# Kernel tuning notes

Hardware: AMD Instinct MI355X
Metric: run time of the kernel (lower is better)

Reference implementation:

```python
import jax, jax.numpy as jnp
import numpy as np

B, S, D, H, DFF = 2, 2048, 768, 12, 3072
HD = D // H
LN_EPS = 1e-5


def _layernorm(x, g, b):
    mu = jnp.mean(x, axis=-1, keepdims=True)
    var = jnp.mean((x - mu) ** 2, axis=-1, keepdims=True)
    return (x - mu) * jax.lax.rsqrt(var + LN_EPS) * g + b


def setup_inputs() -> dict:
    key = jax.random.key(0)
    ks = jax.random.split(key, 16)
    s_d = 1.0 / np.sqrt(D)
    s_ff = 1.0 / np.sqrt(DFF)
    return {
        "x": jax.random.normal(ks[0], (B, S, D), jnp.float32),
        "alibi_bias": jax.random.normal(ks[1], (H, S, S), jnp.float32) * 0.1,
        "Wq": jax.random.normal(ks[2], (D, D), jnp.float32) * s_d,
        "bq": jnp.zeros((D,), jnp.float32),
        "Wk": jax.random.normal(ks[3], (D, D), jnp.float32) * s_d,
        "bk": jnp.zeros((D,), jnp.float32),
        "Wv": jax.random.normal(ks[4], (D, D), jnp.float32) * s_d,
        "bv": jnp.zeros((D,), jnp.float32),
        "Wo": jax.random.normal(ks[5], (D, D), jnp.float32) * s_d,
        "bo": jnp.zeros((D,), jnp.float32),
        "W1": jax.random.normal(ks[6], (D, DFF), jnp.float32) * s_d,
        "b1": jnp.zeros((DFF,), jnp.float32),
        "W2": jax.random.normal(ks[7], (DFF, D), jnp.float32) * s_ff,
        "b2": jnp.zeros((D,), jnp.float32),
        "g1": jnp.ones((D,), jnp.float32),
        "be1": jnp.zeros((D,), jnp.float32),
        "g2": jnp.ones((D,), jnp.float32),
        "be2": jnp.zeros((D,), jnp.float32),
    }


def reference(x, alibi_bias, Wq, bq, Wk, bk, Wv, bv, Wo, bo, W1, b1, W2, b2, g1, be1, g2, be2):
    # QKV projections -> (B, H, S, HD)
    def split_heads(t):
        return t.reshape(B, S, H, HD).transpose(0, 2, 1, 3)

    q = split_heads(x @ Wq + bq)
    k = split_heads(x @ Wk + bk)
    v = split_heads(x @ Wv + bv)

    # causal mask (S, S): -inf above diagonal
    causal = jnp.where(jnp.triu(jnp.ones((S, S), bool), k=1), -jnp.inf, 0.0).astype(x.dtype)
    mask = alibi_bias[None] + causal[None, None]  # (1, H, S, S) broadcast over batch

    scale = 1.0 / np.sqrt(HD)
    scores = jnp.einsum("bhqd,bhkd->bhqk", q, k) * scale + mask
    probs = jax.nn.softmax(scores, axis=-1)
    attn = jnp.einsum("bhqk,bhkd->bhqd", probs, v)  # (B, H, S, HD)
    attn = attn.transpose(0, 2, 1, 3).reshape(B, S, D)
    attn = attn @ Wo + bo

    x = _layernorm(x + attn, g1, be1)
    ff = jax.nn.relu(x @ W1 + b1) @ W2 + b2
    x = _layernorm(x + ff, g2, be2)
    return x
```

## Files before the change

### kernel.cpp

```cpp
#include <hip/hip_runtime.h>
#include <hip/hip_bf16.h>

#define BB 2
#define SS 2048
#define DD 768
#define HH 12
#define HD 64
#define DFF 3072
#define NROW (BB * SS)
#define QLD  2304
#define LN_EPS 1e-5f

typedef __attribute__((ext_vector_type(8))) short bf16x8;
typedef __attribute__((ext_vector_type(4))) short bf16x4;
typedef __attribute__((ext_vector_type(4))) float f32x4;

__device__ __forceinline__ void gll16(const void* g, void* l) {
    __builtin_amdgcn_global_load_lds(
        (const __attribute__((address_space(1))) unsigned int*)g,
        (__attribute__((address_space(3))) unsigned int*)l,
        16, 0, 0);
}

__device__ __forceinline__ unsigned short bf16bits(float f) {
    __hip_bfloat16 h = __float2bfloat16(f);
    return *(unsigned short*)&h;
}

__device__ __forceinline__ float bf16tof(unsigned short u) {
    unsigned int ui = ((unsigned int)u) << 16;
    return __uint_as_float(ui);
}

__device__ __forceinline__ float block_sum(float v, float* red) {
    __syncthreads();
    #pragma unroll
    for (int off = 32; off > 0; off >>= 1) v += __shfl_down(v, off, 64);
    if ((threadIdx.x & 63) == 0) red[threadIdx.x >> 6] = v;
    __syncthreads();
    if (threadIdx.x == 0) red[0] = red[0] + red[1] + red[2] + red[3];
    __syncthreads();
    return red[0];
}

template<int TM, int TN>
__global__ __launch_bounds__(256) void mfma_gemm(
        const __hip_bfloat16* __restrict__ A, const __hip_bfloat16* __restrict__ BT,
        const float* __restrict__ bias, float* __restrict__ Cf,
        __hip_bfloat16* __restrict__ Cb,
        int N, int K, int relu, int bf16out, int qscale_cols) {
    constexpr int BK = 32;
    constexpr int MW = TM / 32;
    constexpr int NW = TN / 32;
    __shared__ __hip_bfloat16 a_s[TM * BK];
    __shared__ __hip_bfloat16 b_s[TN * BK];

    const int tid  = threadIdx.x;
    const int lane = tid & 63;
    const int wid  = tid >> 6;
    const int wm   = (wid & 1) * (TM / 2);
    const int wn   = (wid >> 1) * (TN / 2);
    const int qq   = lane & 15;
    const int quad = lane >> 4;
    const int m0 = blockIdx.y * TM;
    const int n0 = blockIdx.x * TN;

    const int srow = lane >> 2;
    const int scol = (lane & 3) * 8;

    f32x4 acc[MW][NW] = {};

    for (int k0 = 0; k0 < K; k0 += BK) {
        const __hip_bfloat16* Ag = A + (size_t)m0 * K + k0 + scol;
        #pragma unroll
        for (int i = 0; i < TM / 64; i++) {
            const int row = i * 64 + wid * 16 + srow;
            gll16(Ag + (size_t)row * K, a_s + row * BK + scol);
        }
        const __hip_bfloat16* Bg = BT + (size_t)n0 * K + k0 + scol;
        #pragma unroll
        for (int i = 0; i < TN / 64; i++) {
            const int row = i * 64 + wid * 16 + srow;
            gll16(Bg + (size_t)row * K, b_s + row * BK + scol);
        }
        __syncthreads();

        bf16x8 af[MW], bfr[NW];
        #pragma unroll
        for (int mi = 0; mi < MW; mi++)
            af[mi] = *(const bf16x8*)(a_s + (wm + mi * 16 + qq) * BK + quad * 8);
        #pragma unroll
        for (int ni = 0; ni < NW; ni++)
            bfr[ni] = *(const bf16x8*)(b_s + (wn + ni * 16 + qq) * BK + quad * 8);
        #pragma unroll
        for (int mi = 0; mi < MW; mi++)
            #pragma unroll
            for (int ni = 0; ni < NW; ni++)
                acc[mi][ni] = __builtin_amdgcn_mfma_f32_16x16x32_bf16(
                        af[mi], bfr[ni], acc[mi][ni], 0, 0, 0);
        __syncthreads();
    }

    #pragma unroll
    for (int mi = 0; mi < MW; mi++) {
        #pragma unroll
        for (int ni = 0; ni < NW; ni++) {
            const int col = n0 + wn + ni * 16 + qq;
            const float bv = bias[col];
            const float sc = (col < qscale_cols) ? 0.125f : 1.0f;
            #pragma unroll
            for (int r = 0; r < 4; r++) {
                const int row = m0 + wm + mi * 16 + quad * 4 + r;
                float v = acc[mi][ni][r] + bv;
                if (relu) v = fmaxf(v, 0.f);
                v *= sc;
                if (bf16out) Cb[(size_t)row * N + col] = __float2bfloat16(v);
                else         Cf[(size_t)row * N + col] = v;
            }
        }
    }
}

__global__ __launch_bounds__(256) void transpose_bf16_kernel(
        const float* __restrict__ in, __hip_bfloat16* __restrict__ out,
        int K, int N) {
    __shared__ float t[32][33];
    const int n0 = blockIdx.x * 32;
    const int k0 = blockIdx.y * 32;
    const int r = threadIdx.x >> 3;
    const int c = threadIdx.x & 7;
    float4 v = *(const float4*)&in[(size_t)(k0 + r) * N + n0 + c * 4];
    t[r][c * 4 + 0] = v.x;
    t[r][c * 4 + 1] = v.y;
    t[r][c * 4 + 2] = v.z;
    t[r][c * 4 + 3] = v.w;
    __syncthreads();
    union { unsigned short u[4]; uint2 w; } pk;
    #pragma unroll
    for (int j = 0; j < 4; j++) pk.u[j] = bf16bits(t[c * 4 + j][r]);
    *(uint2*)&out[(size_t)(n0 + r) * K + k0 + c * 4] = pk.w;
}

__global__ __launch_bounds__(256) void cvt_bf16_kernel(
        const float* __restrict__ in, __hip_bfloat16* __restrict__ out) {
    const int i = blockIdx.x * 256 + threadIdx.x;
    float4 v = ((const float4*)in)[i];
    union { unsigned short u[4]; uint2 w; } pk;
    pk.u[0] = bf16bits(v.x); pk.u[1] = bf16bits(v.y);
    pk.u[2] = bf16bits(v.z); pk.u[3] = bf16bits(v.w);
    ((uint2*)out)[i] = pk.w;
}

__global__ __launch_bounds__(256) void concat_bias_kernel(
        const float* __restrict__ bq, const float* __restrict__ bk,
        const float* __restrict__ bv, float* __restrict__ o) {
    const int i = blockIdx.x * 256 + threadIdx.x;
    if (i < QLD)
        o[i] = (i < DD) ? bq[i] : ((i < 2 * DD) ? bk[i - DD] : bv[i - 2 * DD]);
}

__global__ __launch_bounds__(256) void flash_attn_kernel(
        const __hip_bfloat16* __restrict__ QKV, const float* __restrict__ alibi,
        __hip_bfloat16* __restrict__ outb) {
    const int qt = (int)gridDim.x - 1 - (int)blockIdx.x;
    const int h  = blockIdx.y;
    const int b  = blockIdx.z;
    const int tid  = threadIdx.x;
    const int lane = tid & 63;
    const int w    = tid >> 6;
    const int qq   = lane & 15;
    const int quad = lane >> 4;
    const int q0   = qt * 64;

    __shared__ unsigned short K_s[64 * 72];
    __shared__ unsigned short V_t[64 * 72];
    __shared__ unsigned short al_q[64 * 72];
    __shared__ unsigned short P_t[4][16 * 72];

    const size_t qrow = ((size_t)(b * SS + q0 + w * 16 + qq)) * QLD + (size_t)h * HD;
    const bf16x8 qf0 = *(const bf16x8*)(QKV + qrow + quad * 8);
    const bf16x8 qf1 = *(const bf16x8*)(QKV + qrow + 32 + quad * 8);

    f32x4 O[4] = {};
    float m_i = -1e30f, l_i = 0.f;

    const float* alrow = alibi + ((size_t)h * SS + q0) * SS;
    const size_t kvrow0 = (size_t)(b * SS) * QLD + (size_t)h * HD + w * 16;
    const int lim = q0 + w * 16 + qq;

    for (int k0 = 0; k0 <= q0; k0 += 64) {
        __syncthreads();

        {
            const size_t kv = kvrow0 + (size_t)(k0 + lane) * QLD;
            bf16x8 kv0 = *(const bf16x8*)(QKV + DD + kv);
            bf16x8 kv1 = *(const bf16x8*)(QKV + DD + kv + 8);
            *(bf16x8*)&K_s[lane * 72 + w * 16]     = kv0;
            *(bf16x8*)&K_s[lane * 72 + w * 16 + 8] = kv1;
            bf16x8 vv0 = *(const bf16x8*)(QKV + 2 * DD + kv);
            bf16x8 vv1 = *(const bf16x8*)(QKV + 2 * DD + kv + 8);
            #pragma unroll
            for (int j = 0; j < 8; j++) {
                V_t[(w * 16 + j) * 72 + lane]     = vv0[j];
                V_t[(w * 16 + 8 + j) * 72 + lane] = vv1[j];
            }
            const float* ap = alrow + (size_t)lane * SS + k0 + w * 16;
            union { unsigned short u[8]; bf16x8 v; } pa0, pa1;
            float4 f0 = *(const float4*)(ap);
            float4 f1 = *(const float4*)(ap + 4);
            float4 f2 = *(const float4*)(ap + 8);
            float4 f3 = *(const float4*)(ap + 12);
            pa0.u[0] = bf16bits(f0.x); pa0.u[1] = bf16bits(f0.y);
            pa0.u[2] = bf16bits(f0.z); pa0.u[3] = bf16bits(f0.w);
            pa0.u[4] = bf16bits(f1.x); pa0.u[5] = bf16bits(f1.y);
            pa0.u[6] = bf16bits(f1.z); pa0.u[7] = bf16bits(f1.w);
            pa1.u[0] = bf16bits(f2.x); pa1.u[1] = bf16bits(f2.y);
            pa1.u[2] = bf16bits(f2.z); pa1.u[3] = bf16bits(f2.w);
            pa1.u[4] = bf16bits(f3.x); pa1.u[5] = bf16bits(f3.y);
            pa1.u[6] = bf16bits(f3.z); pa1.u[7] = bf16bits(f3.w);
            *(bf16x8*)&al_q[lane * 72 + w * 16]     = pa0.v;
            *(bf16x8*)&al_q[lane * 72 + w * 16 + 8] = pa1.v;
        }
        __syncthreads();

        f32x4 S[4];
        #pragma unroll
        for (int c = 0; c < 4; c++) {
            f32x4 s = {};
            bf16x8 kf0 = *(const bf16x8*)&K_s[(c * 16 + qq) * 72 + quad * 8];
            bf16x8 kf1 = *(const bf16x8*)&K_s[(c * 16 + qq) * 72 + 32 + quad * 8];
            s = __builtin_amdgcn_mfma_f32_16x16x32_bf16(kf0, qf0, s, 0, 0, 0);
            s = __builtin_amdgcn_mfma_f32_16x16x32_bf16(kf1, qf1, s, 0, 0, 0);
            S[c] = s;
        }

        float sv[16];
        float smax = -1e30f;
        const int klim = lim - k0;
        #pragma unroll
        for (int c = 0; c < 4; c++) {
            bf16x4 a4 = *(const bf16x4*)&al_q[(w * 16 + qq) * 72 + c * 16 + quad * 4];
            #pragma unroll
            for (int r = 0; r < 4; r++) {
                const int key = c * 16 + quad * 4 + r;
                float s = S[c][r] + bf16tof((unsigned short)a4[r]);
                if (key > klim) s = -1e30f;
                sv[c * 4 + r] = s;
                smax = fmaxf(smax, s);
            }
        }
        smax = fmaxf(smax, __shfl_xor(smax, 16));
        smax = fmaxf(smax, __shfl_xor(smax, 32));

        const float nm = fmaxf(m_i, smax);
        const float alpha = __expf(m_i - nm);
        float lsum = 0.f;
        #pragma unroll
        for (int i = 0; i < 16; i++) {
            const float e = __expf(sv[i] - nm);
            sv[i] = e;
            lsum += e;
        }
        lsum += __shfl_xor(lsum, 16);
        lsum += __shfl_xor(lsum, 32);
        l_i = l_i * alpha + lsum;
        m_i = nm;

        #pragma unroll
        for (int c = 0; c < 4; c++) {
            bf16x4 pk;
            #pragma unroll
            for (int r = 0; r < 4; r++) pk[r] = (short)bf16bits(sv[c * 4 + r]);
            *(bf16x4*)&P_t[w][qq * 72 + c * 16 + quad * 4] = pk;
        }

        #pragma unroll
        for (int r = 0; r < 4; r++) {
            const float ar = __shfl(alpha, quad * 4 + r);
            #pragma unroll
            for (int d = 0; d < 4; d++) O[d][r] *= ar;
        }

        const bf16x8 pf0 = *(const bf16x8*)&P_t[w][qq * 72 + quad * 8];
        const bf16x8 pf1 = *(const bf16x8*)&P_t[w][qq * 72 + 32 + quad * 8];
        #pragma unroll
        for (int d0 = 0; d0 < 4; d0++) {
            bf16x8 vf0 = *(const bf16x8*)&V_t[(d0 * 16 + qq) * 72 + quad * 8];
            bf16x8 vf1 = *(const bf16x8*)&V_t[(d0 * 16 + qq) * 72 + 32 + quad * 8];
            O[d0] = __builtin_amdgcn_mfma_f32_16x16x32_bf16(pf0, vf0, O[d0], 0, 0, 0);
            O[d0] = __builtin_amdgcn_mfma_f32_16x16x32_bf16(pf1, vf1, O[d0], 0, 0, 0);
        }
    }

    const float inv = 1.f / l_i;
    #pragma unroll
    for (int r = 0; r < 4; r++) {
        const float ir = __shfl(inv, quad * 4 + r);
        const int row = q0 + w * 16 + quad * 4 + r;
        __hip_bfloat16* op = outb + (size_t)(b * SS + row) * DD + (size_t)h * HD + qq;
        op[0]  = __float2bfloat16(O[0][r] * ir);
        op[16] = __float2bfloat16(O[1][r] * ir);
        op[32] = __float2bfloat16(O[2][r] * ir);
        op[48] = __float2bfloat16(O[3][r] * ir);
    }
}

__global__ __launch_bounds__(256) void ln_kernel(
        const float* __restrict__ a, const float* __restrict__ r,
        const float* __restrict__ g, const float* __restrict__ beta,
        float* __restrict__ outf, __hip_bfloat16* __restrict__ outb) {
    const int row = blockIdx.x;
    const int tid = threadIdx.x;
    __shared__ float red[64];

    float vals[3];
    float s = 0.f;
    #pragma unroll
    for (int i = 0; i < 3; i++) {
        const int col = i * 256 + tid;
        float t = a[(size_t)row * DD + col] + r[(size_t)row * DD + col];
        vals[i] = t;
        s += t;
    }
    const float mean = block_sum(s, red) * (1.f / DD);

    float s2 = 0.f;
    #pragma unroll
    for (int i = 0; i < 3; i++) {
        float d = vals[i] - mean;
        s2 += d * d;
    }
    const float var = block_sum(s2, red) * (1.f / DD);
    const float rstd = rsqrtf(var + LN_EPS);

    #pragma unroll
    for (int i = 0; i < 3; i++) {
        const int col = i * 256 + tid;
        const float o = (vals[i] - mean) * rstd * g[col] + beta[col];
        outf[(size_t)row * DD + col] = o;
        if (outb) outb[(size_t)row * DD + col] = __float2bfloat16(o);
    }
}

extern "C" void kernel_launch(void* const* d_in, const int* in_sizes, int n_in,
                              void* d_out, int out_size, void* d_ws, size_t ws_size,
                              hipStream_t stream) {
    const float* x     = (const float*)d_in[0];
    const float* alibi = (const float*)d_in[1];
    const float* Wq = (const float*)d_in[2];
    const float* bq = (const float*)d_in[3];
    const float* Wk = (const float*)d_in[4];
    const float* bk = (const float*)d_in[5];
    const float* Wv = (const float*)d_in[6];
    const float* bv = (const float*)d_in[7];
    const float* Wo = (const float*)d_in[8];
    const float* bo = (const float*)d_in[9];
    const float* W1 = (const float*)d_in[10];
    const float* b1 = (const float*)d_in[11];
    const float* W2 = (const float*)d_in[12];
    const float* b2 = (const float*)d_in[13];
    const float* g1 = (const float*)d_in[14];
    const float* be1 = (const float*)d_in[15];
    const float* g2 = (const float*)d_in[16];
    const float* be2 = (const float*)d_in[17];
    float* out = (float*)d_out;

    char* p = (char*)d_ws;
    auto alloc = [&](size_t bytes) { char* r = p; p += (bytes + 255) & ~(size_t)255; return r; };
    __hip_bfloat16* WqkvT = (__hip_bfloat16*)alloc((size_t)QLD * DD * 2);
    __hip_bfloat16* WoT   = (__hip_bfloat16*)alloc((size_t)DD * DD * 2);
    __hip_bfloat16* W1T   = (__hip_bfloat16*)alloc((size_t)DFF * DD * 2);
    __hip_bfloat16* W2T   = (__hip_bfloat16*)alloc((size_t)DD * DFF * 2);
    float*          biasc = (float*)alloc((size_t)QLD * 4);
    __hip_bfloat16* xb    = (__hip_bfloat16*)alloc((size_t)NROW * DD * 2);
    __hip_bfloat16* qkvb  = (__hip_bfloat16*)alloc((size_t)NROW * DFF * 2);
    __hip_bfloat16* attnb = (__hip_bfloat16*)alloc((size_t)NROW * DD * 2);
    float*          proj  = (float*)alloc((size_t)NROW * DD * 4);
    float*          ln1   = (float*)alloc((size_t)NROW * DD * 4);
    __hip_bfloat16* ln1b  = xb;
    __hip_bfloat16* ff1b  = qkvb;
    float*          ff2   = proj;

    const dim3 blk(256);

    transpose_bf16_kernel<<<dim3(DD / 32, DD / 32), blk, 0, stream>>>(Wq, WqkvT, DD, DD);
    transpose_bf16_kernel<<<dim3(DD / 32, DD / 32), blk, 0, stream>>>(Wk, WqkvT + (size_t)DD * DD, DD, DD);
    transpose_bf16_kernel<<<dim3(DD / 32, DD / 32), blk, 0, stream>>>(Wv, WqkvT + (size_t)2 * DD * DD, DD, DD);
    transpose_bf16_kernel<<<dim3(DD / 32, DD / 32), blk, 0, stream>>>(Wo, WoT, DD, DD);
    transpose_bf16_kernel<<<dim3(DFF / 32, DD / 32), blk, 0, stream>>>(W1, W1T, DD, DFF);
    transpose_bf16_kernel<<<dim3(DD / 32, DFF / 32), blk, 0, stream>>>(W2, W2T, DFF, DD);
    concat_bias_kernel<<<dim3((QLD + 255) / 256), blk, 0, stream>>>(bq, bk, bv, biasc);
    cvt_bf16_kernel<<<dim3(NROW * DD / 4 / 256), blk, 0, stream>>>(x, xb);

    mfma_gemm<128, 128><<<dim3(QLD / 128, NROW / 128), blk, 0, stream>>>(
            xb, WqkvT, biasc, nullptr, qkvb, QLD, DD, 0, 1, DD);

    flash_attn_kernel<<<dim3(SS / 64, HH, BB), blk, 0, stream>>>(qkvb, alibi, attnb);

    mfma_gemm<128, 64><<<dim3(DD / 64, NROW / 128), blk, 0, stream>>>(
            attnb, WoT, bo, proj, nullptr, DD, DD, 0, 0, 0);

    ln_kernel<<<dim3(NROW), blk, 0, stream>>>(x, proj, g1, be1, ln1, ln1b);

    mfma_gemm<128, 128><<<dim3(DFF / 128, NROW / 128), blk, 0, stream>>>(
            ln1b, W1T, b1, nullptr, ff1b, DFF, DD, 1, 1, 0);
    mfma_gemm<128, 64><<<dim3(DD / 64, NROW / 128), blk, 0, stream>>>(
            ff1b, W2T, b2, ff2, nullptr, DD, DFF, 0, 0, 0);

    ln_kernel<<<dim3(NROW), blk, 0, stream>>>(ln1, ff2, g2, be2, out, nullptr);
}
```

Baseline: 573.6 us.

## Prefetch next K/V tile into registers and read alibi bias directly

Global loads of K and V for the next key tile are issued into registers before the current tile is computed, which double-buffers through registers and hides global latency behind the MFMA and softmax work. The ALiBi bias is no longer staged through shared memory with a bf16 conversion. Each lane loads its own fp32 bias values straight into registers, which removes the al_q buffer and gives full fp32 bias precision. Barriers become raw s_barrier calls with an explicit lgkmcnt wait. This raises register pressure and makes correctness depend on the hand-placed synchronization.

```diff
diff --git a/kernel.cpp b/kernel.cpp
--- a/kernel.cpp
+++ b/kernel.cpp
@@ -174,7 +174,6 @@
 
     __shared__ unsigned short K_s[64 * 72];
     __shared__ unsigned short V_t[64 * 72];
-    __shared__ unsigned short al_q[64 * 72];
     __shared__ unsigned short P_t[4][16 * 72];
 
     const size_t qrow = ((size_t)(b * SS + q0 + w * 16 + qq)) * QLD + (size_t)h * HD;
@@ -184,44 +183,51 @@
     f32x4 O[4] = {};
     float m_i = -1e30f, l_i = 0.f;
 
-    const float* alrow = alibi + ((size_t)h * SS + q0) * SS;
-    const size_t kvrow0 = (size_t)(b * SS) * QLD + (size_t)h * HD + w * 16;
+    const float* alrow = alibi + ((size_t)h * SS + q0 + w * 16 + qq) * SS;
+    const __hip_bfloat16* Kg = QKV + DD     + (size_t)(b * SS) * QLD + (size_t)h * HD + w * 16;
+    const __hip_bfloat16* Vg = QKV + 2 * DD + (size_t)(b * SS) * QLD + (size_t)h * HD + w * 16;
     const int lim = q0 + w * 16 + qq;
 
+    {
+    }
+    const size_t roff0 = (size_t)lane * QLD;
+    bf16x8 nk0 = *(const bf16x8*)(Kg + roff0);
+    bf16x8 nk1 = *(const bf16x8*)(Kg + roff0 + 8);
+    bf16x8 nv0 = *(const bf16x8*)(Vg + roff0);
+    bf16x8 nv1 = *(const bf16x8*)(Vg + roff0 + 8);
+    float4 na0 = *(const float4*)(alrow + quad * 4);
+    float4 na1 = *(const float4*)(alrow + 16 + quad * 4);
+    float4 na2 = *(const float4*)(alrow + 32 + quad * 4);
+    float4 na3 = *(const float4*)(alrow + 48 + quad * 4);
+
     for (int k0 = 0; k0 <= q0; k0 += 64) {
-        __syncthreads();
-
-        {
-            const size_t kv = kvrow0 + (size_t)(k0 + lane) * QLD;
-            bf16x8 kv0 = *(const bf16x8*)(QKV + DD + kv);
-            bf16x8 kv1 = *(const bf16x8*)(QKV + DD + kv + 8);
-            *(bf16x8*)&K_s[lane * 72 + w * 16]     = kv0;
-            *(bf16x8*)&K_s[lane * 72 + w * 16 + 8] = kv1;
-            bf16x8 vv0 = *(const bf16x8*)(QKV + 2 * DD + kv);
-            bf16x8 vv1 = *(const bf16x8*)(QKV + 2 * DD + kv + 8);
-            #pragma unroll
-            for (int j = 0; j < 8; j++) {
-                V_t[(w * 16 + j) * 72 + lane]     = vv0[j];
-                V_t[(w * 16 + 8 + j) * 72 + lane] = vv1[j];
-            }
-            const float* ap = alrow + (size_t)lane * SS + k0 + w * 16;
-            union { unsigned short u[8]; bf16x8 v; } pa0, pa1;
-            float4 f0 = *(const float4*)(ap);
-            float4 f1 = *(const float4*)(ap + 4);
-            float4 f2 = *(const float4*)(ap + 8);
-            float4 f3 = *(const float4*)(ap + 12);
-            pa0.u[0] = bf16bits(f0.x); pa0.u[1] = bf16bits(f0.y);
-            pa0.u[2] = bf16bits(f0.z); pa0.u[3] = bf16bits(f0.w);
-            pa0.u[4] = bf16bits(f1.x); pa0.u[5] = bf16bits(f1.y);
-            pa0.u[6] = bf16bits(f1.z); pa0.u[7] = bf16bits(f1.w);
-            pa1.u[0] = bf16bits(f2.x); pa1.u[1] = bf16bits(f2.y);
-            pa1.u[2] = bf16bits(f2.z); pa1.u[3] = bf16bits(f2.w);
-            pa1.u[4] = bf16bits(f3.x); pa1.u[5] = bf16bits(f3.y);
-            pa1.u[6] = bf16bits(f3.z); pa1.u[7] = bf16bits(f3.w);
-            *(bf16x8*)&al_q[lane * 72 + w * 16]     = pa0.v;
-            *(bf16x8*)&al_q[lane * 72 + w * 16 + 8] = pa1.v;
-        }
-        __syncthreads();
+        const float4 a0 = na0, a1 = na1, a2 = na2, a3 = na3;
+
+        __builtin_amdgcn_s_barrier();
+
+        *(bf16x8*)&K_s[lane * 72 + w * 16]     = nk0;
+        *(bf16x8*)&K_s[lane * 72 + w * 16 + 8] = nk1;
+        #pragma unroll
+        for (int j = 0; j < 8; j++) {
+            V_t[(w * 16 + j) * 72 + lane]     = nv0[j];
+            V_t[(w * 16 + 8 + j) * 72 + lane] = nv1[j];
+        }
+
+        if (k0 + 64 <= q0) {
+            const size_t nroff = (size_t)(k0 + 64 + lane) * QLD;
+            nk0 = *(const bf16x8*)(Kg + nroff);
+            nk1 = *(const bf16x8*)(Kg + nroff + 8);
+            nv0 = *(const bf16x8*)(Vg + nroff);
+            nv1 = *(const bf16x8*)(Vg + nroff + 8);
+            const float* ap = alrow + k0 + 64;
+            na0 = *(const float4*)(ap + quad * 4);
+            na1 = *(const float4*)(ap + 16 + quad * 4);
+            na2 = *(const float4*)(ap + 32 + quad * 4);
+            na3 = *(const float4*)(ap + 48 + quad * 4);
+        }
+
+        asm volatile("s_waitcnt lgkmcnt(0)" ::: "memory");
+        __builtin_amdgcn_s_barrier();
 
         f32x4 S[4];
         #pragma unroll
@@ -239,11 +245,11 @@
         const int klim = lim - k0;
         #pragma unroll
         for (int c = 0; c < 4; c++) {
-            bf16x4 a4 = *(const bf16x4*)&al_q[(w * 16 + qq) * 72 + c * 16 + quad * 4];
+            const float4 ac = (c == 0) ? a0 : (c == 1) ? a1 : (c == 2) ? a2 : a3;
             #pragma unroll
             for (int r = 0; r < 4; r++) {
                 const int key = c * 16 + quad * 4 + r;
-                float s = S[c][r] + bf16tof((unsigned short)a4[r]);
+                float s = S[c][r] + ((const float*)&ac)[r];
                 if (key > klim) s = -1e30f;
                 sv[c * 4 + r] = s;
                 smax = fmaxf(smax, s);
```

New measurement: 614.7 us. 1.07x slower.

## Split flash attention over key tiles into two partial blocks with combine kernel

Applied to the files above, without the earlier changes.

Each query tile is now processed by two blocks that handle alternating key tiles. Each block writes an unnormalized partial output plus its running max and sum. A new combine kernel merges the two partials with a log-sum-exp rescale. This doubles grid parallelism and shortens the longest causal tiles, easing tail imbalance on many CUs. The cost is an extra kernel launch, partial-output traffic through reused workspace buffers, and bf16 rounding of the unnormalized partials.

```diff
diff --git a/kernel.cpp b/kernel.cpp
--- a/kernel.cpp
+++ b/kernel.cpp
@@ -161,8 +161,9 @@
 
 __global__ __launch_bounds__(256) void flash_attn_kernel(
         const __hip_bfloat16* __restrict__ QKV, const float* __restrict__ alibi,
-        __hip_bfloat16* __restrict__ outb) {
-    const int qt = (int)gridDim.x - 1 - (int)blockIdx.x;
+        __hip_bfloat16* __restrict__ Opart, float* __restrict__ ml) {
+    const int qt = (int)(gridDim.x >> 1) - 1 - (int)(blockIdx.x >> 1);
+    const int s  = blockIdx.x & 1;
     const int h  = blockIdx.y;
     const int b  = blockIdx.z;
     const int tid  = threadIdx.x;
@@ -188,7 +189,8 @@
     const size_t kvrow0 = (size_t)(b * SS) * QLD + (size_t)h * HD + w * 16;
     const int lim = q0 + w * 16 + qq;
 
-    for (int k0 = 0; k0 <= q0; k0 += 64) {
+    for (int t = s; t * 64 <= q0; t += 2) {
+        const int k0 = t * 64;
         __syncthreads();
 
         {
@@ -226,12 +228,12 @@
         f32x4 S[4];
         #pragma unroll
         for (int c = 0; c < 4; c++) {
-            f32x4 s = {};
+            f32x4 sacc = {};
             bf16x8 kf0 = *(const bf16x8*)&K_s[(c * 16 + qq) * 72 + quad * 8];
             bf16x8 kf1 = *(const bf16x8*)&K_s[(c * 16 + qq) * 72 + 32 + quad * 8];
-            s = __builtin_amdgcn_mfma_f32_16x16x32_bf16(kf0, qf0, s, 0, 0, 0);
-            s = __builtin_amdgcn_mfma_f32_16x16x32_bf16(kf1, qf1, s, 0, 0, 0);
-            S[c] = s;
+            sacc = __builtin_amdgcn_mfma_f32_16x16x32_bf16(kf0, qf0, sacc, 0, 0, 0);
+            sacc = __builtin_amdgcn_mfma_f32_16x16x32_bf16(kf1, qf1, sacc, 0, 0, 0);
+            S[c] = sacc;
         }
 
         float sv[16];
@@ -243,10 +245,10 @@
             #pragma unroll
             for (int r = 0; r < 4; r++) {
                 const int key = c * 16 + quad * 4 + r;
-                float s = S[c][r] + bf16tof((unsigned short)a4[r]);
-                if (key > klim) s = -1e30f;
-                sv[c * 4 + r] = s;
-                smax = fmaxf(smax, s);
+                float sc = S[c][r] + bf16tof((unsigned short)a4[r]);
+                if (key > klim) sc = -1e30f;
+                sv[c * 4 + r] = sc;
+                smax = fmaxf(smax, sc);
             }
         }
         smax = fmaxf(smax, __shfl_xor(smax, 16));
@@ -292,17 +294,48 @@
         }
     }
 
-    const float inv = 1.f / l_i;
+    if (quad == 0) {
+        float* mlp = ml + (((size_t)(b * SS + q0 + w * 16 + qq) * HH + h) * 2 + s) * 2;
+        mlp[0] = m_i;
+        mlp[1] = l_i;
+    }
     #pragma unroll
     for (int r = 0; r < 4; r++) {
-        const float ir = __shfl(inv, quad * 4 + r);
         const int row = q0 + w * 16 + quad * 4 + r;
-        __hip_bfloat16* op = outb + (size_t)(b * SS + row) * DD + (size_t)h * HD + qq;
-        op[0]  = __float2bfloat16(O[0][r] * ir);
-        op[16] = __float2bfloat16(O[1][r] * ir);
-        op[32] = __float2bfloat16(O[2][r] * ir);
-        op[48] = __float2bfloat16(O[3][r] * ir);
-    }
+        __hip_bfloat16* op = Opart +
+            (((size_t)(b * SS + row) * HH + h) * 2 + s) * 64 + qq;
+        op[0]  = __float2bfloat16(O[0][r]);
+        op[16] = __float2bfloat16(O[1][r]);
+        op[32] = __float2bfloat16(O[2][r]);
+        op[48] = __float2bfloat16(O[3][r]);
+    }
+}
+
+__global__ __launch_bounds__(256) void attn_combine_kernel(
+        const __hip_bfloat16* __restrict__ Opart, const float* __restrict__ ml,
+        __hip_bfloat16* __restrict__ attnb) {
+    const int idx = blockIdx.x * 256 + threadIdx.x;
+    const int rr  = idx / 96;
+    const int rem = idx - rr * 96;
+    const int h   = rem >> 3;
+    const int d8  = (rem & 7) * 8;
+    const size_t base = ((size_t)rr * HH + h) * 2;
+    const float m0 = ml[(base + 0) * 2], l0 = ml[(base + 0) * 2 + 1];
+    const float m1 = ml[(base + 1) * 2], l1 = ml[(base + 1) * 2 + 1];
+    const float m  = fmaxf(m0, m1);
+    const float e0 = __expf(m0 - m);
+    const float e1 = __expf(m1 - m);
+    const float inv = 1.f / (l0 * e0 + l1 * e1);
+    const bf16x8 o0 = *(const bf16x8*)(Opart + (base + 0) * 64 + d8);
+    const bf16x8 o1 = *(const bf16x8*)(Opart + (base + 1) * 64 + d8);
+    union { unsigned short u[8]; bf16x8 v; } pk;
+    #pragma unroll
+    for (int j = 0; j < 8; j++) {
+        const float v = (bf16tof((unsigned short)o0[j]) * e0 +
+                         bf16tof((unsigned short)o1[j]) * e1) * inv;
+        pk.u[j] = bf16bits(v);
+    }
+    *(bf16x8*)(attnb + (size_t)rr * DD + h * 64 + d8) = pk.v;
 }
 
 __global__ __launch_bounds__(256) void ln_kernel(
@@ -381,6 +414,9 @@
     __hip_bfloat16* ff1b  = qkvb;
     float*          ff2   = proj;
 
+    __hip_bfloat16* Opart = (__hip_bfloat16*)proj;
+    float*          mlbuf = (float*)xb;
+
     const dim3 blk(256);
 
     transpose_bf16_kernel<<<dim3(DD / 32, DD / 32), blk, 0, stream>>>(Wq, WqkvT, DD, DD);
@@ -395,7 +431,10 @@
     mfma_gemm<128, 128><<<dim3(QLD / 128, NROW / 128), blk, 0, stream>>>(
             xb, WqkvT, biasc, nullptr, qkvb, QLD, DD, 0, 1, DD);
 
-    flash_attn_kernel<<<dim3(SS / 64, HH, BB), blk, 0, stream>>>(qkvb, alibi, attnb);
+    flash_attn_kernel<<<dim3(2 * (SS / 64), HH, BB), blk, 0, stream>>>(
+            qkvb, alibi, Opart, mlbuf);
+    attn_combine_kernel<<<dim3(NROW * 96 / 256), blk, 0, stream>>>(
+            Opart, mlbuf, attnb);
 
     mfma_gemm<128, 64><<<dim3(DD / 64, NROW / 128), blk, 0, stream>>>(
             attnb, WoT, bo, proj, nullptr, DD, DD, 0, 0, 0);
```

Result: faster. 557.3 us (-2.8%).
